# Kernel tuning notes

Measured on AMD Instinct MI355X. Metric: run time of the kernel, lower is better.

Reference implementation:

```python
import jax, jax.numpy as jnp
import numpy as np

D_MODEL = 1024
D_STATE = 128
HEAD_DIM = 64
EXPAND = 2
K = 4  # conv_kernel
N_GROUPS = 1
D_INNER = EXPAND * D_MODEL            # 2048
N_HEADS = D_INNER // HEAD_DIM         # 32
D_PROJ = 2 * D_INNER + 2 * N_GROUPS * D_STATE + N_HEADS  # 4384
EPS = 1e-6


def _rmsnorm(x, w):
    return x * jax.lax.rsqrt(jnp.mean(x * x, axis=-1, keepdims=True) + EPS) * w


def setup_inputs() -> dict:
    key = jax.random.key(0)
    ks = jax.random.split(key, 8)
    B, L = 2, 2048
    x = jax.random.normal(ks[0], (B, L, D_MODEL), jnp.float32)
    norm_w = jnp.ones((D_MODEL,), jnp.float32)
    in_proj_w = jax.random.normal(ks[1], (D_PROJ, D_MODEL), jnp.float32) / np.sqrt(D_MODEL).astype(np.float32)
    conv_w = jax.random.normal(ks[2], (D_INNER, K), jnp.float32) / np.sqrt(K).astype(np.float32)
    conv_b = jnp.zeros((D_INNER,), jnp.float32)
    A_log = jnp.log(jax.random.uniform(ks[3], (N_HEADS,), jnp.float32) * 15.0 + 1.0)
    D = jnp.ones((N_HEADS,), jnp.float32)
    dt_bias = jnp.log(jax.random.uniform(ks[4], (N_HEADS,), jnp.float32) * 0.099 + 0.001)
    out_proj_w = jax.random.normal(ks[5], (D_MODEL, D_INNER), jnp.float32) / np.sqrt(D_INNER).astype(np.float32)
    return dict(x=x, norm_w=norm_w, in_proj_w=in_proj_w, conv_w=conv_w, conv_b=conv_b,
                A_log=A_log, D=D, dt_bias=dt_bias, out_proj_w=out_proj_w)


def reference(x, norm_w, in_proj_w, conv_w, conv_b, A_log, D, dt_bias, out_proj_w):
    batch, L, _ = x.shape
    residual = x
    xn = _rmsnorm(x, norm_w)
    proj = jnp.einsum('bld,pd->blp', xn, in_proj_w)  # (B,L,D_PROJ)

    # split fused projection -> z, x_ssm, B, C, dt_raw
    i = 0
    z = proj[:, :, i:i + D_INNER]; i += D_INNER
    x_ssm = proj[:, :, i:i + D_INNER]; i += D_INNER
    bc = N_GROUPS * D_STATE
    Bm = proj[:, :, i:i + bc].reshape(batch, L, N_GROUPS, D_STATE); i += bc
    Cm = proj[:, :, i:i + bc].reshape(batch, L, N_GROUPS, D_STATE); i += bc
    dt_raw = proj[:, :, i:i + N_HEADS]

    # causal depthwise conv1d (left-pad K-1) + SiLU
    xp = jnp.pad(x_ssm, ((0, 0), (K - 1, 0), (0, 0)))
    x_conv = conv_b
    for k in range(K):
        x_conv = x_conv + xp[:, k:k + L, :] * conv_w[:, k]
    x_conv = jax.nn.silu(x_conv)

    xh = x_conv.reshape(batch, L, N_HEADS, HEAD_DIM)
    dt = jax.nn.softplus(dt_raw + dt_bias)          # (B,L,H)
    dA = jnp.exp(-jnp.exp(A_log) * dt)              # (B,L,H)
    dtx = dt[..., None] * xh                        # (B,L,H,P)

    gidx = jnp.arange(N_HEADS) // (N_HEADS // N_GROUPS)
    Bg = Bm[:, :, gidx, :]                          # (B,L,H,N)
    Cg = Cm[:, :, gidx, :]                          # (B,L,H,N)

    def step(h, inp):
        dA_t, dtx_t, B_t, C_t = inp                 # (B,H), (B,H,P), (B,H,N), (B,H,N)
        h = h * dA_t[:, :, None, None] + dtx_t[..., None] * B_t[:, :, None, :]
        y_t = jnp.einsum('bhpn,bhn->bhp', h, C_t)
        return h, y_t

    h0 = jnp.zeros((batch, N_HEADS, HEAD_DIM, D_STATE), jnp.float32)
    xs = (jnp.swapaxes(dA, 0, 1), jnp.swapaxes(dtx, 0, 1),
          jnp.swapaxes(Bg, 0, 1), jnp.swapaxes(Cg, 0, 1))
    _, ys = jax.lax.scan(step, h0, xs)              # ys: (L,B,H,P)
    y = jnp.swapaxes(ys, 0, 1) + D[None, None, :, None] * xh

    y = y.reshape(batch, L, D_INNER) * jax.nn.silu(z)
    return residual + jnp.einsum('bli,di->bld', y, out_proj_w)
```

## Files before the change

### kernel.cpp

```cpp
#include <hip/hip_runtime.h>
#include <hip/hip_bf16.h>

#define L_SEQ 2048
#define DM 1024
#define DI 2048
#define DS 128
#define NH 32
#define HD 64
#define DPROJ 4384
#define DPAD 4480
#define NBATCH 2
#define NCH 8
#define CH 256
#define B_OFF 4096
#define C_OFF 4224
#define DT_OFF 4352
#define SWZ(row) ((((row) ^ ((row) >> 3)) & 7) << 4)

typedef unsigned short u16;
typedef __attribute__((ext_vector_type(8))) short short8;
typedef __attribute__((ext_vector_type(4))) float f32x4;

#define GLL16(g, l)                                                     \
  __builtin_amdgcn_global_load_lds(                                     \
      (const __attribute__((address_space(1))) unsigned int*)(g),       \
      (__attribute__((address_space(3))) unsigned int*)(l), 16, 0, 0)
#define SBAR __builtin_amdgcn_s_barrier()
#define MEMFENCE asm volatile("" ::: "memory")

__device__ __forceinline__ u16 f2bf(float f) {
  union { float f; unsigned u; } c; c.f = f;
  unsigned u = c.u;
  u += 0x7fffu + ((u >> 16) & 1u);
  return (u16)(u >> 16);
}
__device__ __forceinline__ float bf2f(u16 u) {
  return __uint_as_float((unsigned)u << 16);
}
__device__ __forceinline__ float siluf(float x) {
  return x / (1.0f + expf(-x));
}
__device__ __forceinline__ void store_out(u16* C, size_t o, float v) { C[o] = f2bf(v); }
__device__ __forceinline__ void store_out(float* C, size_t o, float v) { C[o] = v; }

__global__ __launch_bounds__(256) void prep_kernel(
    const float* __restrict__ x, const float* __restrict__ norm_w,
    const float* __restrict__ w1, const float* __restrict__ w2,
    u16* __restrict__ xnb, u16* __restrict__ w1b, u16* __restrict__ w2b,
    int M) {
  int bidx = blockIdx.x;
  int t = threadIdx.x;
  if (bidx < M) {
    const float* row = x + (size_t)bidx * DM;
    float4 v = *(const float4*)(row + t * 4);
    float ss = v.x * v.x + v.y * v.y + v.z * v.z + v.w * v.w;
#pragma unroll
    for (int o = 32; o > 0; o >>= 1) ss += __shfl_xor(ss, o);
    __shared__ float sred[4];
    if ((t & 63) == 0) sred[t >> 6] = ss;
    __syncthreads();
    ss = sred[0] + sred[1] + sred[2] + sred[3];
    float rs = rsqrtf(ss * (1.0f / DM) + 1e-6f);
    float4 wv = *(const float4*)(norm_w + t * 4);
    ushort4 o;
    o.x = f2bf(v.x * rs * wv.x);
    o.y = f2bf(v.y * rs * wv.y);
    o.z = f2bf(v.z * rs * wv.z);
    o.w = f2bf(v.w * rs * wv.w);
    *(ushort4*)(xnb + (size_t)bidx * DM + t * 4) = o;
  } else if (bidx < M + DPAD) {
    int r = bidx - M;
    int c = t * 4;
    ushort4 u;
    if (r < DPROJ) {
      float4 v = *(const float4*)(w1 + (size_t)r * DM + c);
      u.x = f2bf(v.x); u.y = f2bf(v.y); u.z = f2bf(v.z); u.w = f2bf(v.w);
    } else {
      u.x = 0; u.y = 0; u.z = 0; u.w = 0;
    }
    *(ushort4*)(w1b + (size_t)r * DM + c) = u;
  } else {
    size_t i = ((size_t)(bidx - M - DPAD) * 256 + t) * 8;
    float4 v0 = *(const float4*)(w2 + i);
    float4 v1 = *(const float4*)(w2 + i + 4);
    ushort4 a, b;
    a.x = f2bf(v0.x); a.y = f2bf(v0.y); a.z = f2bf(v0.z); a.w = f2bf(v0.w);
    b.x = f2bf(v1.x); b.y = f2bf(v1.y); b.z = f2bf(v1.z); b.w = f2bf(v1.w);
    *(ushort4*)(w2b + i) = a;
    *(ushort4*)(w2b + i + 4) = b;
  }
}

template <typename OT, bool RES, bool DTS, int BN>
__global__ __launch_bounds__(256, 4) void gemm_bt(
    const u16* __restrict__ A, const u16* __restrict__ Bw,
    OT* __restrict__ C, const float* __restrict__ resid,
    float* __restrict__ dts, int M, int N, int K, int nbx) {
  constexpr int WN = BN / 2;
  constexpr int NJ = WN / 16;
  __shared__ u16 lA[3][128 * 32];
  __shared__ u16 lB[3][BN * 32];
  const int tid = threadIdx.x;
  const int wv = tid >> 6, lane = tid & 63;
  const int wm = wv >> 1, wn = wv & 1;

  const int nwg = gridDim.x;
  const int cpx = nwg >> 3;
  const int wg = blockIdx.x;
  const int swz = (wg & 7) * cpx + (wg >> 3);
  const int m0 = (swz / nbx) * 128, n0 = (swz % nbx) * BN;

  const int rowS = tid >> 2;
  const int colS = (tid & 3) * 8;
  const u16* gA0 = A + (size_t)(m0 + rowS) * K + colS;
  const u16* gA1 = A + (size_t)(m0 + rowS + 64) * K + colS;
  const u16* gB0 = Bw + (size_t)(n0 + rowS) * K + colS;
  const u16* gB1 = Bw + (size_t)(n0 + rowS + 64) * K + colS;

  auto stage = [&](int kt, int buf) {
    const int ko = kt << 5;
    GLL16(gA0 + ko, &lA[buf][wv * 512]);
    GLL16(gA1 + ko, &lA[buf][2048 + wv * 512]);
    GLL16(gB0 + ko, &lB[buf][wv * 512]);
    if (BN == 128) GLL16(gB1 + ko, &lB[buf][2048 + wv * 512]);
  };

  f32x4 acc[4][NJ] = {};
  const int r = lane & 15;
  const int koff = (lane >> 4) * 8;

  auto compute = [&](int buf) {
    short8 af[4], bfr[NJ];
#pragma unroll
    for (int i = 0; i < 4; ++i)
      af[i] = *(const short8*)&lA[buf][(wm * 64 + i * 16 + r) * 32 + koff];
#pragma unroll
    for (int j = 0; j < NJ; ++j)
      bfr[j] = *(const short8*)&lB[buf][(wn * WN + j * 16 + r) * 32 + koff];
#pragma unroll
    for (int i = 0; i < 4; ++i)
#pragma unroll
      for (int j = 0; j < NJ; ++j)
        acc[i][j] = __builtin_amdgcn_mfma_f32_16x16x32_bf16(
            af[i], bfr[j], acc[i][j], 0, 0, 0);
  };

  const int nk = K >> 5;
  stage(0, 0);
  stage(1, 1);
  int cur = 0;
  for (int kt = 0; kt < nk; ++kt) {
    if (kt + 1 < nk) {
      if (BN == 128) asm volatile("s_waitcnt vmcnt(4)" ::: "memory");
      else           asm volatile("s_waitcnt vmcnt(3)" ::: "memory");
    } else {
      asm volatile("s_waitcnt vmcnt(0)" ::: "memory");
    }
    SBAR;
    MEMFENCE;
    if (kt + 2 < nk) {
      int nb = cur + 2; if (nb >= 3) nb -= 3;
      stage(kt + 2, nb);
    }
    compute(cur);
    ++cur; if (cur == 3) cur = 0;
  }

  const int rbase = m0 + wm * 64 + (lane >> 4) * 4;
  const int cbase = n0 + wn * WN + (lane & 15);
#pragma unroll
  for (int i = 0; i < 4; ++i) {
#pragma unroll
    for (int j = 0; j < NJ; ++j) {
      int row0 = rbase + i * 16;
      int col = cbase + j * 16;
#pragma unroll
      for (int rr = 0; rr < 4; ++rr) {
        size_t o = (size_t)(row0 + rr) * N + col;
        float v = acc[i][j][rr];
        if (RES) v += resid[o];
        store_out(C, o, v);
        if (DTS) {
          if (col >= DT_OFF && col < DT_OFF + NH)
            dts[(size_t)(row0 + rr) * NH + (col - DT_OFF)] = v;
        }
      }
    }
  }
}

__global__ __launch_bounds__(256) void convdt_kernel(
    const u16* __restrict__ proj, const float* __restrict__ cw,
    const float* __restrict__ cb, u16* __restrict__ xh,
    const float* __restrict__ dts, const float* __restrict__ dt_bias,
    const float* __restrict__ A_log, float* __restrict__ dAdt, int M) {
  int bidx = blockIdx.x;
  if (bidx < M) {
    int m = bidx;
    int l = m & (L_SEQ - 1);
    int c0 = threadIdx.x * 8;
    float4 wv[8];
#pragma unroll
    for (int j = 0; j < 8; ++j) wv[j] = *(const float4*)(cw + (size_t)(c0 + j) * 4);
    float acc[8];
#pragma unroll
    for (int j = 0; j < 8; ++j) acc[j] = cb[c0 + j];
#pragma unroll
    for (int k = 0; k < 4; ++k) {
      int lk = l + k - 3;
      if (lk >= 0) {
        short8 rv8 = *(const short8*)(proj + (size_t)(m + k - 3) * DPAD + DI + c0);
#pragma unroll
        for (int j = 0; j < 8; ++j) {
          float wk = (k == 0) ? wv[j].x : (k == 1) ? wv[j].y : (k == 2) ? wv[j].z : wv[j].w;
          acc[j] = fmaf(bf2f((u16)rv8[j]), wk, acc[j]);
        }
      }
    }
    short8 o;
#pragma unroll
    for (int j = 0; j < 8; ++j) o[j] = (short)f2bf(siluf(acc[j]));
    *(short8*)(xh + (size_t)m * DI + c0) = o;
  } else {
    int idx = (bidx - M) * 256 + threadIdx.x;
    int h = idx & 31;
    float raw = dts[idx] + dt_bias[h];
    float dt = fmaxf(raw, 0.0f) + log1pf(expf(-fabsf(raw)));
    float a = -expf(A_log[h]) * dt;
    float2 o; o.x = a; o.y = dt;
    *(float2*)(dAdt + (size_t)idx * 2) = o;
  }
}

__global__ __launch_bounds__(512) void scan_state_mfma(
    const u16* __restrict__ proj, const float* __restrict__ dAdt,
    const u16* __restrict__ xhy, float* __restrict__ S,
    float* __restrict__ P) {
  __shared__ u16 sBT[128 * 64];
  __shared__ u16 sXT[64 * 64];
  __shared__ u16 sXW[64 * 64];
  __shared__ float sDt[64], sCum[64], sWs[64], sLam[64];

  const int bid = blockIdx.x;
  const int ch = bid & 7, hh = (bid >> 3) & 31, b = bid >> 8;
  const int tid = threadIdx.x;
  const int w = tid >> 6, l = tid & 63;
  const int tw = w >> 1, half = w & 1;
  const int klane = (l >> 4) * 16;
  const size_t mchunk = (size_t)(b * L_SEQ + ch * CH);

  f32x4 hAcc[4] = {};
  float ctot = 0.0f;

  auto STAGE = [&](int sc) {
    const size_t m0 = mchunk + (size_t)sc * 64;
    {
      const int tp = tid >> 4;
      const int n0 = (tid & 15) * 8;
      const u16* r0 = proj + (m0 + 2 * tp) * DPAD + B_OFF + n0;
      short8 lo8 = *(const short8*)r0;
      short8 hi8 = *(const short8*)(r0 + DPAD);
#pragma unroll
      for (int q = 0; q < 8; ++q) {
        int n = n0 + q;
        unsigned v = (unsigned)(u16)lo8[q] | ((unsigned)(u16)hi8[q] << 16);
        *(unsigned*)((char*)sBT + ((n * 128 + 4 * tp) ^ SWZ(n))) = v;
      }
    }
    {
      const int sx = tid >> 3;
      const int p0 = (tid & 7) * 8;
      short8 xv8 = *(const short8*)(xhy + (m0 + sx) * DI + hh * 64 + p0);
#pragma unroll
      for (int i = 0; i < 8; ++i) {
        int p = p0 + i;
        *(u16*)((char*)sXT + ((p * 128 + 2 * sx) ^ SWZ(p))) = (u16)xv8[i];
      }
    }
    if (tid < 64) {
      float2 ad = *(const float2*)(dAdt + (m0 + tid) * 64 + hh * 2);
      float a = ad.x, dtv = ad.y;
      sDt[tid] = dtv;
      float val = a;
#pragma unroll
      for (int o = 1; o < 64; o <<= 1) {
        float t2 = __shfl_up(val, o);
        if (tid >= o) val += t2;
      }
      sCum[tid] = val;
      float c63 = __shfl(val, 63);
      sWs[tid] = __expf(c63 - val) * dtv;
      sLam[tid] = __expf(val);
    }
  };

  STAGE(0);
  __syncthreads();

  for (int sc = 0; sc < 4; ++sc) {
    {
      int p = tid >> 3, sg = tid & 7;
      int byteX = (p * 128 + sg * 16) ^ SWZ(p);
      short8 xv = *(short8*)((char*)sXT + byteX);
      short8 outp;
#pragma unroll
      for (int j = 0; j < 8; ++j)
        outp[j] = (short)f2bf(bf2f((u16)xv[j]) * sWs[sg * 8 + j]);
      *(short8*)((char*)sXW + byteX) = outp;
    }
    __syncthreads();

    {
      float lam63 = sLam[63];
      ctot += sCum[63];
#pragma unroll
      for (int j = 0; j < 4; ++j) {
        hAcc[j][0] *= lam63; hAcc[j][1] *= lam63;
        hAcc[j][2] *= lam63; hAcc[j][3] *= lam63;
      }
      int prow = tw * 16 + (l & 15);
      short8 aXW[2];
#pragma unroll
      for (int kk = 0; kk < 2; ++kk)
        aXW[kk] = *(short8*)((char*)sXW + ((prow * 128 + kk * 64 + klane) ^ SWZ(prow)));
#pragma unroll
      for (int j = 0; j < 4; ++j) {
        int nrow = (half * 4 + j) * 16 + (l & 15);
#pragma unroll
        for (int kk = 0; kk < 2; ++kk) {
          short8 bBT = *(short8*)((char*)sBT + ((nrow * 128 + kk * 64 + klane) ^ SWZ(nrow)));
          hAcc[j] = __builtin_amdgcn_mfma_f32_16x16x32_bf16(aXW[kk], bBT, hAcc[j], 0, 0, 0);
        }
      }
    }
    __syncthreads();
    if (sc < 3) STAGE(sc + 1);
    __syncthreads();
  }

  float* Sb = S + (size_t)((b * 32 + hh) * NCH + ch) * 8192;
  const int p0 = tw * 16 + (l >> 4) * 4;
#pragma unroll
  for (int j = 0; j < 4; ++j) {
    int n = (half * 4 + j) * 16 + (l & 15);
#pragma unroll
    for (int r = 0; r < 4; ++r)
      Sb[(p0 + r) * 128 + n] = hAcc[j][r];
  }
  if (tid == 0) P[(b * 32 + hh) * NCH + ch] = __expf(ctot);
}

__global__ __launch_bounds__(256) void combine_kernel(
    float* __restrict__ S, const float* __restrict__ P) {
  int tid = blockIdx.x * 256 + threadIdx.x;
  int bh = tid >> 13, pn = tid & 8191;
  size_t base = (size_t)bh * NCH * 8192 + pn;
  float E = 0.0f;
#pragma unroll
  for (int c = 0; c < NCH; ++c) {
    size_t o = base + (size_t)c * 8192;
    float Sc = S[o];
    S[o] = E;
    E = fmaf(P[bh * NCH + c], E, Sc);
  }
}

__global__ __launch_bounds__(512) void scan_y_mfma(
    const u16* __restrict__ proj, const float* __restrict__ dAdt,
    const u16* __restrict__ xhy, const float* __restrict__ Dv,
    const float* __restrict__ S, u16* __restrict__ yb) {
  __shared__ u16 sC[64 * 128];
  __shared__ u16 sB[64 * 128];
  __shared__ u16 sHb[64 * 128];
  __shared__ u16 sBT[128 * 64];
  __shared__ u16 sXT[64 * 64];
  __shared__ u16 sXW[64 * 64];
  __shared__ u16 sW[64 * 64];
  __shared__ float sDt[64], sCum[64], sWs[64], sLam[64];

  const int bid = blockIdx.x;
  const int ch = bid & 7, hh = (bid >> 3) & 31, b = bid >> 8;
  const int tid = threadIdx.x;
  const int w = tid >> 6, l = tid & 63;
  const int tw = w >> 1, half = w & 1;
  const int klane = (l >> 4) * 16;
  const float Dh = Dv[hh];
  const size_t mchunk = (size_t)(b * L_SEQ + ch * CH);

  f32x4 hAcc[4];
  {
    const float* Sb = S + (size_t)((b * 32 + hh) * NCH + ch) * 8192;
    const int p0 = tw * 16 + (l >> 4) * 4;
#pragma unroll
    for (int j = 0; j < 4; ++j) {
      int n = (half * 4 + j) * 16 + (l & 15);
#pragma unroll
      for (int r = 0; r < 4; ++r)
        hAcc[j][r] = Sb[(p0 + r) * 128 + n];
    }
    int p = tid >> 3, sg = tid & 7;
#pragma unroll
    for (int i = 0; i < 4; ++i) {
      float4 v = *(const float4*)(Sb + p * 128 + sg * 16 + 4 * i);
      ushort4 u;
      u.x = f2bf(v.x); u.y = f2bf(v.y); u.z = f2bf(v.z); u.w = f2bf(v.w);
      *(ushort4*)((char*)sHb + ((p * 256 + (sg * 16 + 4 * i) * 2) ^ SWZ(p))) = u;
    }
  }

  auto STAGE = [&](int sc) {
    const size_t m0 = mchunk + (size_t)sc * 64;
    {
      const int tp = tid >> 4;
      const int n0 = (tid & 15) * 8;
      const u16* r0 = proj + (m0 + 2 * tp) * DPAD;
      short8 b0 = *(const short8*)(r0 + B_OFF + n0);
      short8 b1 = *(const short8*)(r0 + DPAD + B_OFF + n0);
      short8 c0v = *(const short8*)(r0 + C_OFF + n0);
      short8 c1v = *(const short8*)(r0 + DPAD + C_OFF + n0);
      *(short8*)((char*)sB + ((2 * tp * 256 + n0 * 2) ^ SWZ(2 * tp))) = b0;
      *(short8*)((char*)sB + (((2 * tp + 1) * 256 + n0 * 2) ^ SWZ(2 * tp + 1))) = b1;
      *(short8*)((char*)sC + ((2 * tp * 256 + n0 * 2) ^ SWZ(2 * tp))) = c0v;
      *(short8*)((char*)sC + (((2 * tp + 1) * 256 + n0 * 2) ^ SWZ(2 * tp + 1))) = c1v;
#pragma unroll
      for (int q = 0; q < 8; ++q) {
        int n = n0 + q;
        unsigned v = (unsigned)(u16)b0[q] | ((unsigned)(u16)b1[q] << 16);
        *(unsigned*)((char*)sBT + ((n * 128 + 4 * tp) ^ SWZ(n))) = v;
      }
    }
    {
      const int sx = tid >> 3;
      const int p0 = (tid & 7) * 8;
      short8 xv8 = *(const short8*)(xhy + (m0 + sx) * DI + hh * 64 + p0);
#pragma unroll
      for (int i = 0; i < 8; ++i) {
        int p = p0 + i;
        *(u16*)((char*)sXT + ((p * 128 + 2 * sx) ^ SWZ(p))) = (u16)xv8[i];
      }
    }
    if (tid < 64) {
      float2 ad = *(const float2*)(dAdt + (m0 + tid) * 64 + hh * 2);
      float a = ad.x, dtv = ad.y;
      sDt[tid] = dtv;
      float val = a;
#pragma unroll
      for (int o = 1; o < 64; o <<= 1) {
        float t2 = __shfl_up(val, o);
        if (tid >= o) val += t2;
      }
      sCum[tid] = val;
      float c63 = __shfl(val, 63);
      sWs[tid] = __expf(c63 - val) * dtv;
      sLam[tid] = __expf(val);
    }
  };

  STAGE(0);
  __syncthreads();

  for (int sc = 0; sc < 4; ++sc) {
    const size_t m0 = mchunk + (size_t)sc * 64;
    {
      int p = tid >> 3, sg = tid & 7;
      int byteX = (p * 128 + sg * 16) ^ SWZ(p);
      short8 xv = *(short8*)((char*)sXT + byteX);
      short8 outp;
#pragma unroll
      for (int j = 0; j < 8; ++j)
        outp[j] = (short)f2bf(bf2f((u16)xv[j]) * sWs[sg * 8 + j]);
      *(short8*)((char*)sXW + byteX) = outp;
    }
    __syncthreads();

    const int trow = tw * 16 + (l & 15);
    short8 aC[4];
#pragma unroll
    for (int kk = 0; kk < 4; ++kk)
      aC[kk] = *(short8*)((char*)sC + ((trow * 256 + kk * 64 + klane) ^ SWZ(trow)));

    {
      f32x4 g[2] = {};
#pragma unroll
      for (int sv2 = 0; sv2 < 2; ++sv2) {
        int srow = (half * 2 + sv2) * 16 + (l & 15);
#pragma unroll
        for (int kk = 0; kk < 4; ++kk) {
          short8 bB = *(short8*)((char*)sB + ((srow * 256 + kk * 64 + klane) ^ SWZ(srow)));
          g[sv2] = __builtin_amdgcn_mfma_f32_16x16x32_bf16(aC[kk], bB, g[sv2], 0, 0, 0);
        }
      }
#pragma unroll
      for (int sv2 = 0; sv2 < 2; ++sv2) {
        int s = (half * 2 + sv2) * 16 + (l & 15);
        float dts_ = sDt[s], cums = sCum[s];
#pragma unroll
        for (int r = 0; r < 4; ++r) {
          int t = tw * 16 + (l >> 4) * 4 + r;
          float v = (t >= s) ? g[sv2][r] * __expf(sCum[t] - cums) * dts_ : 0.0f;
          *(u16*)((char*)sW + ((t * 128 + 2 * s) ^ SWZ(t))) = f2bf(v);
        }
      }
    }
    __syncthreads();

    f32x4 y1[2] = {}, y2[2] = {};
    float lamv[4], lam63 = sLam[63];
#pragma unroll
    for (int r = 0; r < 4; ++r) lamv[r] = sLam[tw * 16 + (l >> 4) * 4 + r];
    {
      short8 aW[2];
#pragma unroll
      for (int kk = 0; kk < 2; ++kk)
        aW[kk] = *(short8*)((char*)sW + ((trow * 128 + kk * 64 + klane) ^ SWZ(trow)));
#pragma unroll
      for (int pv2 = 0; pv2 < 2; ++pv2) {
        int prow = (half * 2 + pv2) * 16 + (l & 15);
#pragma unroll
        for (int kk = 0; kk < 2; ++kk) {
          short8 bX = *(short8*)((char*)sXT + ((prow * 128 + kk * 64 + klane) ^ SWZ(prow)));
          y1[pv2] = __builtin_amdgcn_mfma_f32_16x16x32_bf16(aW[kk], bX, y1[pv2], 0, 0, 0);
        }
#pragma unroll
        for (int kk = 0; kk < 4; ++kk) {
          short8 bH = *(short8*)((char*)sHb + ((prow * 256 + kk * 64 + klane) ^ SWZ(prow)));
          y2[pv2] = __builtin_amdgcn_mfma_f32_16x16x32_bf16(aC[kk], bH, y2[pv2], 0, 0, 0);
        }
      }
#pragma unroll
      for (int j = 0; j < 4; ++j) {
        hAcc[j][0] *= lam63; hAcc[j][1] *= lam63;
        hAcc[j][2] *= lam63; hAcc[j][3] *= lam63;
      }
      short8 aXW[2];
#pragma unroll
      for (int kk = 0; kk < 2; ++kk)
        aXW[kk] = *(short8*)((char*)sXW + ((trow * 128 + kk * 64 + klane) ^ SWZ(trow)));
#pragma unroll
      for (int j = 0; j < 4; ++j) {
        int nrow = (half * 4 + j) * 16 + (l & 15);
#pragma unroll
        for (int kk = 0; kk < 2; ++kk) {
          short8 bBT = *(short8*)((char*)sBT + ((nrow * 128 + kk * 64 + klane) ^ SWZ(nrow)));
          hAcc[j] = __builtin_amdgcn_mfma_f32_16x16x32_bf16(aXW[kk], bBT, hAcc[j], 0, 0, 0);
        }
      }
    }
    __syncthreads();

    {
#pragma unroll
      for (int j = 0; j < 4; ++j) {
        int n = (half * 4 + j) * 16 + (l & 15);
#pragma unroll
        for (int r = 0; r < 4; ++r) {
          int p = tw * 16 + (l >> 4) * 4 + r;
          *(u16*)((char*)sHb + ((p * 256 + 2 * n) ^ SWZ(p))) = f2bf(hAcc[j][r]);
        }
      }
#pragma unroll
      for (int pv2 = 0; pv2 < 2; ++pv2) {
        int p = (half * 2 + pv2) * 16 + (l & 15);
#pragma unroll
        for (int r = 0; r < 4; ++r) {
          int t = tw * 16 + (l >> 4) * 4 + r;
          int col = hh * 64 + p;
          size_t gy = (m0 + t) * DI + col;
          float xv = bf2f(xhy[gy]);
          float yv = y1[pv2][r] + lamv[r] * y2[pv2][r] + Dh * xv;
          float zv = bf2f(proj[(m0 + t) * DPAD + col]);
          yb[gy] = f2bf(yv * siluf(zv));
        }
      }
      if (sc < 3) STAGE(sc + 1);
    }
    __syncthreads();
  }
}

extern "C" void kernel_launch(void* const* d_in, const int* in_sizes, int n_in,
                              void* d_out, int out_size, void* d_ws, size_t ws_size,
                              hipStream_t stream) {
  const float* x      = (const float*)d_in[0];
  const float* norm_w = (const float*)d_in[1];
  const float* w1     = (const float*)d_in[2];
  const float* cw     = (const float*)d_in[3];
  const float* cb     = (const float*)d_in[4];
  const float* A_log  = (const float*)d_in[5];
  const float* Dv     = (const float*)d_in[6];
  const float* dt_b   = (const float*)d_in[7];
  const float* w2     = (const float*)d_in[8];
  float* out = (float*)d_out;

  char* ws = (char*)d_ws;
  u16*   xnb  = (u16*)(ws);
  u16*   w1b  = (u16*)(ws + 8388608);
  u16*   w2b  = (u16*)(ws + 17563648);
  u16*   proj = (u16*)(ws + 21757952);
  float* dts  = (float*)(ws + 58458112);
  u16*   xhy  = (u16*)(ws + 58982400);
  float* dAdt = (float*)(ws + 75759616);
  u16*   yb   = (u16*)(ws + 76808192);
  float* S    = (float*)(ws + 93585408);
  float* P    = (float*)(ws + 110362624);

  const int M = NBATCH * L_SEQ;

  prep_kernel<<<M + DPAD + 1024, 256, 0, stream>>>(
      x, norm_w, w1, w2, xnb, w1b, w2b, M);
  gemm_bt<u16, false, true, 128><<<(DPAD / 128) * (M / 128), 256, 0, stream>>>(
      xnb, w1b, proj, nullptr, dts, M, DPAD, DM, DPAD / 128);
  convdt_kernel<<<M + M / 8, 256, 0, stream>>>(
      proj, cw, cb, xhy, dts, dt_b, A_log, dAdt, M);
  scan_state_mfma<<<512, 512, 0, stream>>>(proj, dAdt, xhy, S, P);
  combine_kernel<<<2048, 256, 0, stream>>>(S, P);
  scan_y_mfma<<<512, 512, 0, stream>>>(proj, dAdt, xhy, Dv, S, yb);
  gemm_bt<float, true, false, 64><<<(DM / 64) * (M / 128), 256, 0, stream>>>(
      yb, w2b, out, x, nullptr, M, DM, DI, DM / 64);
}
```

Baseline: 205.0 us.

## Fuse conv/dt into scan kernel, split-K out-proj, double-buffer GEMM

Removes the separate conv+dt kernel and computes the causal conv, SiLU and softplus/dA inside scan_state_mfma, still writing xhy and dAdt for later kernels. The out-projection GEMM becomes split-K by two: it writes two fp32 partials into a workspace, and a new add kernel sums them with the residual. The GEMM pipeline also drops from triple to double buffering with a full vmcnt(0) wait each iteration, which may expose load latency. Split-K doubles the out-proj grid for better occupancy, at the cost of extra partial-sum traffic and one more launch.

```diff
diff --git a/kernel.cpp b/kernel.cpp
--- a/kernel.cpp
+++ b/kernel.cpp
@@ -91,15 +91,15 @@
   }
 }
 
-template <typename OT, bool RES, bool DTS, int BN>
+template <typename OT, bool RES, bool DTS, int BN, int SPLIT>
 __global__ __launch_bounds__(256, 4) void gemm_bt(
     const u16* __restrict__ A, const u16* __restrict__ Bw,
     OT* __restrict__ C, const float* __restrict__ resid,
-    float* __restrict__ dts, int M, int N, int K, int nbx) {
+    float* __restrict__ dts, int M, int N, int Kloop, int LDA, int nbx) {
   constexpr int WN = BN / 2;
   constexpr int NJ = WN / 16;
-  __shared__ u16 lA[3][128 * 32];
-  __shared__ u16 lB[3][BN * 32];
+  __shared__ u16 lA[2][128 * 32];
+  __shared__ u16 lB[2][BN * 32];
   const int tid = threadIdx.x;
   const int wv = tid >> 6, lane = tid & 63;
   const int wm = wv >> 1, wn = wv & 1;
@@ -108,14 +108,20 @@
   const int cpx = nwg >> 3;
   const int wg = blockIdx.x;
   const int swz = (wg & 7) * cpx + (wg >> 3);
-  const int m0 = (swz / nbx) * 128, n0 = (swz % nbx) * BN;
+  int kh = 0, tile = swz;
+  if (SPLIT == 2) { kh = swz & 1; tile = swz >> 1; }
+  const int m0 = (tile / nbx) * 128, n0 = (tile % nbx) * BN;
+
+  const u16* Ab = A + (size_t)kh * Kloop;
+  const u16* Bb = Bw + (size_t)kh * Kloop;
+  OT* Cb = (SPLIT == 2) ? (C + (size_t)kh * M * N) : C;
 
   const int rowS = tid >> 2;
   const int colS = (tid & 3) * 8;
-  const u16* gA0 = A + (size_t)(m0 + rowS) * K + colS;
-  const u16* gA1 = A + (size_t)(m0 + rowS + 64) * K + colS;
-  const u16* gB0 = Bw + (size_t)(n0 + rowS) * K + colS;
-  const u16* gB1 = Bw + (size_t)(n0 + rowS + 64) * K + colS;
+  const u16* gA0 = Ab + (size_t)(m0 + rowS) * LDA + colS;
+  const u16* gA1 = Ab + (size_t)(m0 + rowS + 64) * LDA + colS;
+  const u16* gB0 = Bb + (size_t)(n0 + rowS) * LDA + colS;
+  const u16* gB1 = Bb + (size_t)(n0 + rowS + 64) * LDA + colS;
 
   auto stage = [&](int kt, int buf) {
     const int ko = kt << 5;
@@ -145,25 +151,15 @@
             af[i], bfr[j], acc[i][j], 0, 0, 0);
   };
 
-  const int nk = K >> 5;
+  const int nk = Kloop >> 5;
   stage(0, 0);
-  stage(1, 1);
-  int cur = 0;
   for (int kt = 0; kt < nk; ++kt) {
-    if (kt + 1 < nk) {
-      if (BN == 128) asm volatile("s_waitcnt vmcnt(4)" ::: "memory");
-      else           asm volatile("s_waitcnt vmcnt(3)" ::: "memory");
-    } else {
-      asm volatile("s_waitcnt vmcnt(0)" ::: "memory");
-    }
+    const int b = kt & 1;
+    asm volatile("s_waitcnt vmcnt(0)" ::: "memory");
     SBAR;
     MEMFENCE;
-    if (kt + 2 < nk) {
-      int nb = cur + 2; if (nb >= 3) nb -= 3;
-      stage(kt + 2, nb);
-    }
-    compute(cur);
-    ++cur; if (cur == 3) cur = 0;
+    if (kt + 1 < nk) stage(kt + 1, b ^ 1);
+    compute(b);
   }
 
   const int rbase = m0 + wm * 64 + (lane >> 4) * 4;
@@ -179,7 +175,7 @@
         size_t o = (size_t)(row0 + rr) * N + col;
         float v = acc[i][j][rr];
         if (RES) v += resid[o];
-        store_out(C, o, v);
+        store_out(Cb, o, v);
         if (DTS) {
           if (col >= DT_OFF && col < DT_OFF + NH)
             dts[(size_t)(row0 + rr) * NH + (col - DT_OFF)] = v;
@@ -189,53 +185,29 @@
   }
 }
 
-__global__ __launch_bounds__(256) void convdt_kernel(
-    const u16* __restrict__ proj, const float* __restrict__ cw,
-    const float* __restrict__ cb, u16* __restrict__ xh,
-    const float* __restrict__ dts, const float* __restrict__ dt_bias,
-    const float* __restrict__ A_log, float* __restrict__ dAdt, int M) {
-  int bidx = blockIdx.x;
-  if (bidx < M) {
-    int m = bidx;
-    int l = m & (L_SEQ - 1);
-    int c0 = threadIdx.x * 8;
-    float4 wv[8];
-#pragma unroll
-    for (int j = 0; j < 8; ++j) wv[j] = *(const float4*)(cw + (size_t)(c0 + j) * 4);
-    float acc[8];
-#pragma unroll
-    for (int j = 0; j < 8; ++j) acc[j] = cb[c0 + j];
-#pragma unroll
-    for (int k = 0; k < 4; ++k) {
-      int lk = l + k - 3;
-      if (lk >= 0) {
-        short8 rv8 = *(const short8*)(proj + (size_t)(m + k - 3) * DPAD + DI + c0);
-#pragma unroll
-        for (int j = 0; j < 8; ++j) {
-          float wk = (k == 0) ? wv[j].x : (k == 1) ? wv[j].y : (k == 2) ? wv[j].z : wv[j].w;
-          acc[j] = fmaf(bf2f((u16)rv8[j]), wk, acc[j]);
-        }
-      }
-    }
-    short8 o;
-#pragma unroll
-    for (int j = 0; j < 8; ++j) o[j] = (short)f2bf(siluf(acc[j]));
-    *(short8*)(xh + (size_t)m * DI + c0) = o;
-  } else {
-    int idx = (bidx - M) * 256 + threadIdx.x;
-    int h = idx & 31;
-    float raw = dts[idx] + dt_bias[h];
-    float dt = fmaxf(raw, 0.0f) + log1pf(expf(-fabsf(raw)));
-    float a = -expf(A_log[h]) * dt;
-    float2 o; o.x = a; o.y = dt;
-    *(float2*)(dAdt + (size_t)idx * 2) = o;
+__global__ __launch_bounds__(256) void add_out_kernel(
+    const float* __restrict__ x, const float* __restrict__ p,
+    float* __restrict__ out) {
+  size_t i = ((size_t)blockIdx.x * 256 + threadIdx.x) * 8;
+  const float* p1 = p + (size_t)4096 * 1024;
+#pragma unroll
+  for (int q = 0; q < 2; ++q) {
+    float4 a = *(const float4*)(x + i + q * 4);
+    float4 b = *(const float4*)(p + i + q * 4);
+    float4 c = *(const float4*)(p1 + i + q * 4);
+    float4 o;
+    o.x = a.x + b.x + c.x; o.y = a.y + b.y + c.y;
+    o.z = a.z + b.z + c.z; o.w = a.w + b.w + c.w;
+    *(float4*)(out + i + q * 4) = o;
   }
 }
 
 __global__ __launch_bounds__(512) void scan_state_mfma(
-    const u16* __restrict__ proj, const float* __restrict__ dAdt,
-    const u16* __restrict__ xhy, float* __restrict__ S,
-    float* __restrict__ P) {
+    const u16* __restrict__ proj, const float* __restrict__ dts,
+    const float* __restrict__ dt_bias, const float* __restrict__ A_log,
+    const float* __restrict__ cw, const float* __restrict__ cb,
+    u16* __restrict__ xhy, float* __restrict__ dAdt,
+    float* __restrict__ S, float* __restrict__ P) {
   __shared__ u16 sBT[128 * 64];
   __shared__ u16 sXT[64 * 64];
   __shared__ u16 sXW[64 * 64];
@@ -249,6 +221,17 @@
   const int klane = (l >> 4) * 16;
   const size_t mchunk = (size_t)(b * L_SEQ + ch * CH);
 
+  const int cvp0 = (tid & 7) * 8;
+  float4 cwv[8];
+  float cbv[8];
+#pragma unroll
+  for (int j = 0; j < 8; ++j) {
+    cwv[j] = *(const float4*)(cw + (size_t)(hh * 64 + cvp0 + j) * 4);
+    cbv[j] = cb[hh * 64 + cvp0 + j];
+  }
+  const float dtb_h = dt_bias[hh];
+  const float eAh = expf(A_log[hh]);
+
   f32x4 hAcc[4] = {};
   float ctot = 0.0f;
 
@@ -269,17 +252,40 @@
     }
     {
       const int sx = tid >> 3;
-      const int p0 = (tid & 7) * 8;
-      short8 xv8 = *(const short8*)(xhy + (m0 + sx) * DI + hh * 64 + p0);
+      const int gm = (int)m0 + sx;
+      const int lrow = gm & (L_SEQ - 1);
+      float accv[8];
+#pragma unroll
+      for (int j = 0; j < 8; ++j) accv[j] = cbv[j];
+#pragma unroll
+      for (int k = 0; k < 4; ++k) {
+        if (lrow + k >= 3) {
+          short8 rv = *(const short8*)(proj + (size_t)(gm + k - 3) * DPAD + DI +
+                                       hh * 64 + cvp0);
+#pragma unroll
+          for (int j = 0; j < 8; ++j) {
+            float wk = (k == 0) ? cwv[j].x : (k == 1) ? cwv[j].y
+                      : (k == 2) ? cwv[j].z : cwv[j].w;
+            accv[j] = fmaf(bf2f((u16)rv[j]), wk, accv[j]);
+          }
+        }
+      }
+      short8 o;
 #pragma unroll
       for (int i = 0; i < 8; ++i) {
-        int p = p0 + i;
-        *(u16*)((char*)sXT + ((p * 128 + 2 * sx) ^ SWZ(p))) = (u16)xv8[i];
-      }
+        u16 bv = f2bf(siluf(accv[i]));
+        o[i] = (short)bv;
+        int p = cvp0 + i;
+        *(u16*)((char*)sXT + ((p * 128 + 2 * sx) ^ SWZ(p))) = bv;
+      }
+      *(short8*)(xhy + (size_t)gm * DI + hh * 64 + cvp0) = o;
     }
     if (tid < 64) {
-      float2 ad = *(const float2*)(dAdt + (m0 + tid) * 64 + hh * 2);
-      float a = ad.x, dtv = ad.y;
+      float raw = dts[(m0 + tid) * NH + hh] + dtb_h;
+      float dtv = fmaxf(raw, 0.0f) + log1pf(expf(-fabsf(raw)));
+      float a = -eAh * dtv;
+      float2 ad; ad.x = a; ad.y = dtv;
+      *(float2*)(dAdt + (m0 + tid) * 64 + hh * 2) = ad;
       sDt[tid] = dtv;
       float val = a;
 #pragma unroll
@@ -602,19 +608,20 @@
   float* dAdt = (float*)(ws + 75759616);
   u16*   yb   = (u16*)(ws + 76808192);
   float* S    = (float*)(ws + 93585408);
-  float* P    = (float*)(ws + 110362624);
+  float* part = (float*)(ws + 93585408);
+  float* P    = (float*)(ws + 127139840);
 
   const int M = NBATCH * L_SEQ;
 
   prep_kernel<<<M + DPAD + 1024, 256, 0, stream>>>(
       x, norm_w, w1, w2, xnb, w1b, w2b, M);
-  gemm_bt<u16, false, true, 128><<<(DPAD / 128) * (M / 128), 256, 0, stream>>>(
-      xnb, w1b, proj, nullptr, dts, M, DPAD, DM, DPAD / 128);
-  convdt_kernel<<<M + M / 8, 256, 0, stream>>>(
-      proj, cw, cb, xhy, dts, dt_b, A_log, dAdt, M);
-  scan_state_mfma<<<512, 512, 0, stream>>>(proj, dAdt, xhy, S, P);
+  gemm_bt<u16, false, true, 128, 1><<<(DPAD / 128) * (M / 128), 256, 0, stream>>>(
+      xnb, w1b, proj, nullptr, dts, M, DPAD, DM, DM, DPAD / 128);
+  scan_state_mfma<<<512, 512, 0, stream>>>(
+      proj, dts, dt_b, A_log, cw, cb, xhy, dAdt, S, P);
   combine_kernel<<<2048, 256, 0, stream>>>(S, P);
   scan_y_mfma<<<512, 512, 0, stream>>>(proj, dAdt, xhy, Dv, S, yb);
-  gemm_bt<float, true, false, 64><<<(DM / 64) * (M / 128), 256, 0, stream>>>(
-      yb, w2b, out, x, nullptr, M, DM, DI, DM / 64);
-}
+  gemm_bt<float, false, false, 64, 2><<<2 * (DM / 64) * (M / 128), 256, 0, stream>>>(
+      yb, w2b, part, nullptr, nullptr, M, DM, DI / 2, DI, DM / 64);
+  add_out_kernel<<<M * DM / 2048, 256, 0, stream>>>(x, part, out);
+}
```

Measured after the change: 192.9 us. -5.9%, faster.
